# Performance work log

Hardware: AMD Instinct MI355X
Metric: run time of the kernel (lower is better)

The kernel has to match this reference:

```python
import jax, jax.numpy as jnp
import numpy as np

B, N, D = 2, 2048, 1024
H, WS = 16, 128  # num_heads, window_size
DH = D // H
HALF = WS // 2  # window is [i-HALF, i+HALF] inclusive -> 129 keys interior


def setup_inputs() -> dict:
    key = jax.random.key(0)
    ks = jax.random.split(key, 5)
    return {
        "x": jax.random.normal(ks[0], (B, N, D), dtype=jnp.float32),
        "Wqkv": jax.random.normal(ks[1], (D, 3 * D), dtype=jnp.float32) * 0.02,
        "bqkv": jax.random.normal(ks[2], (3 * D,), dtype=jnp.float32) * 0.02,
        "Wout": jax.random.normal(ks[3], (D, D), dtype=jnp.float32) * 0.02,
        "bout": jax.random.normal(ks[4], (D,), dtype=jnp.float32) * 0.02,
    }


def reference(x, Wqkv, bqkv, Wout, bout):
    b, n, d = x.shape
    scale = DH ** -0.5
    qkv = x @ Wqkv + bqkv  # [b, n, 3d]
    q, k, v = jnp.split(qkv, 3, axis=-1)
    # [b, n, d] -> [b, h, n, dh]
    def heads(t):
        return t.reshape(b, n, H, DH).transpose(0, 2, 1, 3)
    q, k, v = heads(q), heads(k), heads(v)
    scores = jnp.einsum("bhid,bhjd->bhij", q, k) * scale  # [b, h, n, n]
    # per-token window [max(0,i-HALF), min(n,i+HALF+1)) == |i-j| <= HALF
    idx = jnp.arange(n)
    band = jnp.abs(idx[:, None] - idx[None, :]) <= HALF  # [n, n]
    neg = jnp.asarray(jnp.finfo(scores.dtype).min, scores.dtype)
    scores = jnp.where(band[None, None], scores, neg)
    attn = jax.nn.softmax(scores, axis=-1)
    out = jnp.einsum("bhij,bhjd->bhid", attn, v)  # [b, h, n, dh]
    out = out.transpose(0, 2, 1, 3).reshape(b, n, d)
    return out @ Wout + bout
```

## Files before the change

kernel.cpp:

```cpp
#include <hip/hip_runtime.h>
#include <hip/hip_bf16.h>
#include <cstdint>
#include <cstddef>

#define BB 2
#define NN 2048
#define DD 1024
#define HH 16
#define DHH 64
#define SCALE 0.125f

typedef _Float16 f16x8 __attribute__((ext_vector_type(8)));
typedef _Float16 f16x4 __attribute__((ext_vector_type(4)));
typedef float f32x4 __attribute__((ext_vector_type(4)));

#define AS1(p) ((__attribute__((address_space(1))) void*)(p))
#define AS3(p) ((__attribute__((address_space(3))) void*)(p))

__global__ __launch_bounds__(256) void prep(const float* __restrict__ x, _Float16* __restrict__ x_h,
                                            const float* __restrict__ Wqkv, _Float16* __restrict__ Wqkv_t,
                                            const float* __restrict__ Wout, _Float16* __restrict__ Wout_t) {
    __shared__ float tile[32][33];
    int bx = blockIdx.x, tid = threadIdx.x;
    if (bx < 2048) {
        int i = bx * 2048 + tid * 8;
        f32x4 a = *(const f32x4*)(x + i);
        f32x4 b = *(const f32x4*)(x + i + 4);
        f16x8 o;
        o[0] = (_Float16)a[0]; o[1] = (_Float16)a[1]; o[2] = (_Float16)a[2]; o[3] = (_Float16)a[3];
        o[4] = (_Float16)b[0]; o[5] = (_Float16)b[1]; o[6] = (_Float16)b[2]; o[7] = (_Float16)b[3];
        *(f16x8*)(x_h + i) = o;
        return;
    }
    const float* in; _Float16* out; int C, tc, tr;
    if (bx < 5120) { int t = bx - 2048; C = 3 * DD; in = Wqkv; out = Wqkv_t; tc = t % 96; tr = t / 96; }
    else           { int t = bx - 5120; C = DD;     in = Wout; out = Wout_t; tc = t % 32; tr = t / 32; }
    int R = DD;
    int txx = tid & 31, ty = tid >> 5;
    int r0 = tr * 32, c0 = tc * 32;
#pragma unroll
    for (int i = 0; i < 32; i += 8)
        tile[ty + i][txx] = in[(size_t)(r0 + ty + i) * C + (c0 + txx)];
    __syncthreads();
#pragma unroll
    for (int i = 0; i < 32; i += 8)
        out[(size_t)(c0 + ty + i) * R + (r0 + txx)] = (_Float16)tile[txx][ty + i];
}

template <bool SWAP, int MT>
__device__ __forceinline__ void gemm_kloop(const _Float16* __restrict__ gA,
                                           const _Float16* __restrict__ gB,
                                           _Float16* lA, _Float16* lB,
                                           const _Float16* As, const _Float16* Bs,
                                           int wm, int wn, int llo, int lhi, int K,
                                           f32x4 acc[][MT > 4 ? MT : 4]) {
    for (int k0 = 0; k0 < K; k0 += 64) {
        __syncthreads();
#pragma unroll
        for (int p = 0; p < MT; ++p)
            __builtin_amdgcn_global_load_lds(AS1(gA + (size_t)p * 8 * K + k0), AS3(lA + p * 512), 16, 0, 0);
#pragma unroll
        for (int p = 0; p < 4; ++p)
            __builtin_amdgcn_global_load_lds(AS1(gB + (size_t)p * 8 * K + k0), AS3(lB + p * 512), 16, 0, 0);
        __syncthreads();

#pragma unroll
        for (int ks = 0; ks < 2; ++ks) {
            f16x8 af[MT], bf[4];
            int swz = (((ks * 4 + lhi) ^ (llo & 7)) * 8);
#pragma unroll
            for (int mt = 0; mt < MT; ++mt)
                af[mt] = *(const f16x8*)(As + (wm + mt * 16 + llo) * 64 + swz);
#pragma unroll
            for (int nt = 0; nt < 4; ++nt)
                bf[nt] = *(const f16x8*)(Bs + (wn + nt * 16 + llo) * 64 + swz);
            if (SWAP) {
#pragma unroll
                for (int nt = 0; nt < 4; ++nt)
#pragma unroll
                    for (int mt = 0; mt < MT; ++mt)
                        acc[nt][mt] = __builtin_amdgcn_mfma_f32_16x16x32_f16(bf[nt], af[mt], acc[nt][mt], 0, 0, 0);
            } else {
#pragma unroll
                for (int mt = 0; mt < MT; ++mt)
#pragma unroll
                    for (int nt = 0; nt < 4; ++nt)
                        acc[mt][nt] = __builtin_amdgcn_mfma_f32_16x16x32_f16(af[mt], bf[nt], acc[mt][nt], 0, 0, 0);
            }
        }
    }
}

template <bool SWAP>
__device__ __forceinline__ void qkv_body(const _Float16* __restrict__ A,
                                         const _Float16* __restrict__ Bt,
                                         const float* __restrict__ bias,
                                         _Float16* __restrict__ q_h,
                                         _Float16* __restrict__ k_h,
                                         _Float16* __restrict__ vt_h,
                                         _Float16* As, _Float16* Bs,
                                         int bm, int bn, int region) {
    (void)region;
    int tid = threadIdx.x;
    int wave = tid >> 6, lane = tid & 63;
    int llo = lane & 15, lhi = lane >> 4;
    int wm = (wave >> 2) * 128, wn = (wave & 3) * 64;
    int l8 = lane >> 3;
    int gchunk = ((lane & 7) ^ l8) * 8;

    int rAu = wm + (wave & 3) * 16;
    int rBu = (wave >> 1) * 64 + (wave & 1) * 16;
    const _Float16* gA = A + (size_t)(bm + rAu + l8) * DD + gchunk;
    const _Float16* gB = Bt + (size_t)(bn + rBu + l8) * DD + gchunk;
    _Float16* lA = As + rAu * 64 + lane * 8;
    _Float16* lB = Bs + rBu * 64 + lane * 8;

#define STA(H, C, T, U) __builtin_amdgcn_global_load_lds( \
        AS1(gA + (size_t)((H) * 64 + (C) * 8) * DD + (T) * 64), \
        AS3(lA + (U) * 16384 + ((H) * 64 + (C) * 8) * 64), 16, 0, 0)
#define STB(H, C, T, U) __builtin_amdgcn_global_load_lds( \
        AS1(gB + (size_t)((H) * 32 + (C) * 8) * DD + (T) * 64), \
        AS3(lB + (U) * 16384 + ((H) * 32 + (C) * 8) * 64), 16, 0, 0)
#define RDA(MT, KS, U) (*(const f16x8*)(As + (U) * 16384 + (wm + (MT) * 16 + llo) * 64 + ((((KS) * 4 + lhi) ^ (llo & 7)) * 8)))
#define RDB(NT, KS, U) (*(const f16x8*)(Bs + (U) * 16384 + (wn + (NT) * 16 + llo) * 64 + ((((KS) * 4 + lhi) ^ (llo & 7)) * 8)))
#define MM(MT, NT, KS) do { \
        if constexpr (SWAP) acc[NT][MT] = __builtin_amdgcn_mfma_f32_16x16x32_f16(bf[NT][KS], af[(MT) & 3][KS], acc[NT][MT], 0, 0, 0); \
        else acc[MT][NT] = __builtin_amdgcn_mfma_f32_16x16x32_f16(af[(MT) & 3][KS], bf[NT][KS], acc[MT][NT], 0, 0, 0); \
    } while (0)

    f32x4 acc[SWAP ? 4 : 8][SWAP ? 8 : 4] = {};
    f16x8 af[4][2], bf[4][2];

    STA(0, 0, 0, 0); STA(0, 1, 0, 0);
    STB(0, 0, 0, 0); STB(0, 1, 0, 0);
    STB(1, 0, 0, 0); STB(1, 1, 0, 0);
    STA(1, 0, 0, 0); STA(1, 1, 0, 0);
    asm volatile("s_waitcnt vmcnt(4)" ::: "memory");
    __builtin_amdgcn_s_barrier();

#pragma unroll 1
    for (int t = 0; t < 15; ++t) {
        int u = t & 1, nu = u ^ 1;
#pragma unroll
        for (int mt = 0; mt < 4; ++mt) { af[mt][0] = RDA(mt, 0, u); af[mt][1] = RDA(mt, 1, u); }
#pragma unroll
        for (int nt = 0; nt < 2; ++nt) { bf[nt][0] = RDB(nt, 0, u); bf[nt][1] = RDB(nt, 1, u); }
        STA(0, 0, t + 1, nu); STA(0, 1, t + 1, nu);
        STB(0, 0, t + 1, nu); STB(0, 1, t + 1, nu);
        __builtin_amdgcn_s_barrier();
        asm volatile("s_waitcnt lgkmcnt(0)" ::: "memory");
        __builtin_amdgcn_s_setprio(1);
#pragma unroll
        for (int ks = 0; ks < 2; ++ks)
#pragma unroll
            for (int mt = 0; mt < 4; ++mt) { MM(mt, 0, ks); MM(mt, 1, ks); }
        __builtin_amdgcn_s_setprio(0);
        asm volatile("s_waitcnt vmcnt(6)" ::: "memory");
        __builtin_amdgcn_s_barrier();
#pragma unroll
        for (int nt = 2; nt < 4; ++nt) { bf[nt][0] = RDB(nt, 0, u); bf[nt][1] = RDB(nt, 1, u); }
        STB(1, 0, t + 1, nu); STB(1, 1, t + 1, nu);
        __builtin_amdgcn_s_barrier();
        asm volatile("s_waitcnt lgkmcnt(0)" ::: "memory");
        __builtin_amdgcn_s_setprio(1);
#pragma unroll
        for (int ks = 0; ks < 2; ++ks)
#pragma unroll
            for (int mt = 0; mt < 4; ++mt) { MM(mt, 2, ks); MM(mt, 3, ks); }
        __builtin_amdgcn_s_setprio(0);
        asm volatile("s_waitcnt vmcnt(6)" ::: "memory");
        __builtin_amdgcn_s_barrier();
#pragma unroll
        for (int mt = 0; mt < 4; ++mt) { af[mt][0] = RDA(mt + 4, 0, u); af[mt][1] = RDA(mt + 4, 1, u); }
        STA(1, 0, t + 1, nu); STA(1, 1, t + 1, nu);
        __builtin_amdgcn_s_barrier();
        asm volatile("s_waitcnt lgkmcnt(0)" ::: "memory");
        __builtin_amdgcn_s_setprio(1);
#pragma unroll
        for (int ks = 0; ks < 2; ++ks)
#pragma unroll
            for (int mt = 4; mt < 8; ++mt) { MM(mt, 2, ks); MM(mt, 3, ks); }
        __builtin_amdgcn_s_setprio(0);
        __builtin_amdgcn_s_barrier();
        __builtin_amdgcn_s_setprio(1);
#pragma unroll
        for (int ks = 0; ks < 2; ++ks)
#pragma unroll
            for (int mt = 4; mt < 8; ++mt) { MM(mt, 0, ks); MM(mt, 1, ks); }
        __builtin_amdgcn_s_setprio(0);
        asm volatile("s_waitcnt vmcnt(4)" ::: "memory");
        __builtin_amdgcn_s_barrier();
    }

    {
#pragma unroll
        for (int mt = 0; mt < 4; ++mt) { af[mt][0] = RDA(mt, 0, 1); af[mt][1] = RDA(mt, 1, 1); }
#pragma unroll
        for (int nt = 0; nt < 2; ++nt) { bf[nt][0] = RDB(nt, 0, 1); bf[nt][1] = RDB(nt, 1, 1); }
        asm volatile("s_waitcnt lgkmcnt(0)" ::: "memory");
        __builtin_amdgcn_s_setprio(1);
#pragma unroll
        for (int ks = 0; ks < 2; ++ks)
#pragma unroll
            for (int mt = 0; mt < 4; ++mt) { MM(mt, 0, ks); MM(mt, 1, ks); }
        __builtin_amdgcn_s_setprio(0);
        asm volatile("s_waitcnt vmcnt(2)" ::: "memory");
        __builtin_amdgcn_s_barrier();
#pragma unroll
        for (int nt = 2; nt < 4; ++nt) { bf[nt][0] = RDB(nt, 0, 1); bf[nt][1] = RDB(nt, 1, 1); }
        asm volatile("s_waitcnt lgkmcnt(0)" ::: "memory");
        __builtin_amdgcn_s_setprio(1);
#pragma unroll
        for (int ks = 0; ks < 2; ++ks)
#pragma unroll
            for (int mt = 0; mt < 4; ++mt) { MM(mt, 2, ks); MM(mt, 3, ks); }
        __builtin_amdgcn_s_setprio(0);
        asm volatile("s_waitcnt vmcnt(0)" ::: "memory");
        __builtin_amdgcn_s_barrier();
#pragma unroll
        for (int mt = 0; mt < 4; ++mt) { af[mt][0] = RDA(mt + 4, 0, 1); af[mt][1] = RDA(mt + 4, 1, 1); }
        asm volatile("s_waitcnt lgkmcnt(0)" ::: "memory");
        __builtin_amdgcn_s_setprio(1);
#pragma unroll
        for (int ks = 0; ks < 2; ++ks)
#pragma unroll
            for (int mt = 4; mt < 8; ++mt) { MM(mt, 0, ks); MM(mt, 1, ks); MM(mt, 2, ks); MM(mt, 3, ks); }
        __builtin_amdgcn_s_setprio(0);
    }

    if constexpr (SWAP) {
        _Float16* dst0 = (region == 0 ? q_h : k_h);
#pragma unroll
        for (int nt = 0; nt < 4; ++nt) {
            int cbase = bn + wn + nt * 16 + lhi * 4;
            f32x4 b4 = *(const f32x4*)(bias + cbase);
            int c = cbase & 1023;
#pragma unroll
            for (int mt = 0; mt < 8; ++mt) {
                int tkn = bm + wm + mt * 16 + llo;
                int b = tkn >> 11, n = tkn & 2047;
                f16x4 v4;
#pragma unroll
                for (int r = 0; r < 4; ++r) v4[r] = (_Float16)(acc[nt][mt][r] + b4[r]);
                *(f16x4*)(dst0 + (size_t)(b * NN + n) * DD + c) = v4;
            }
        }
    } else {
#pragma unroll
        for (int nt = 0; nt < 4; ++nt) {
            int col = bn + wn + nt * 16 + llo;
            float bv = bias[col];
            int c = col & 1023;
            int h = c >> 6, dh = c & 63;
#pragma unroll
            for (int mt = 0; mt < 8; ++mt) {
                int row = bm + wm + mt * 16 + lhi * 4;
                int b = row >> 11, n = row & 2047;
                f16x4 v4;
#pragma unroll
                for (int r = 0; r < 4; ++r) v4[r] = (_Float16)(acc[mt][nt][r] + bv);
                *(f16x4*)(vt_h + ((size_t)((b * HH + h) * DHH + dh)) * NN + n) = v4;
            }
        }
    }
#undef STA
#undef STB
#undef RDA
#undef RDB
#undef MM
}

__global__ __launch_bounds__(512, 2) void gemm_qkv(const _Float16* __restrict__ A,
                                                   const _Float16* __restrict__ Bt,
                                                   const float* __restrict__ bias,
                                                   _Float16* __restrict__ q_h,
                                                   _Float16* __restrict__ k_h,
                                                   _Float16* __restrict__ vt_h) {
    __shared__ __align__(16) _Float16 As[2 * 16384];
    __shared__ __align__(16) _Float16 Bs[2 * 16384];
    int id = blockIdx.x;
    int xcd = id & 7, jj = id >> 3;
    int mtile = (xcd >> 1) * 4 + jj / 6;
    int ntile = (xcd & 1) * 6 + jj % 6;
    int bm = mtile * 256, bn = ntile * 256;
    int region = bn >> 10;
    if (region == 2)
        qkv_body<false>(A, Bt, bias, q_h, k_h, vt_h, As, Bs, bm, bn, region);
    else
        qkv_body<true>(A, Bt, bias, q_h, k_h, vt_h, As, Bs, bm, bn, region);
}

__global__ __launch_bounds__(256) void gemm_out(const _Float16* __restrict__ A,
                                                const _Float16* __restrict__ Bt,
                                                const float* __restrict__ bias,
                                                float* __restrict__ Cf) {
    const int K = DD, N = DD;
    __shared__ __align__(16) _Float16 As[64 * 64];
    __shared__ __align__(16) _Float16 Bs[128 * 64];
    int id = blockIdx.x;
    int xcd = id & 7, j = id >> 3;
    int bm = (xcd * 8 + (j >> 3)) * 64;
    int bn = (j & 7) * 128;
    int tid = threadIdx.x;
    int wave = tid >> 6, lane = tid & 63;
    int wm = (wave >> 1) * 32, wn = (wave & 1) * 64;
    int lhi = lane >> 4, llo = lane & 15;

    f32x4 acc[4][4] = {};

    int srowA = wave * 16 + (lane >> 3);
    int srowB = wave * 32 + (lane >> 3);
    int scol = ((lane & 7) ^ (lane >> 3)) * 8;
    const _Float16* gA = A + (size_t)(bm + srowA) * K + scol;
    const _Float16* gB = Bt + (size_t)(bn + srowB) * K + scol;
    _Float16* lA = As + wave * 1024 + lane * 8;
    _Float16* lB = Bs + wave * 2048 + lane * 8;

    gemm_kloop<true, 2>(gA, gB, lA, lB, As, Bs, wm, wn, llo, lhi, K,
                        (f32x4(*)[4])acc);

#pragma unroll
    for (int nt = 0; nt < 4; ++nt) {
        int cbase = bn + wn + nt * 16 + lhi * 4;
        f32x4 b4 = *(const f32x4*)(bias + cbase);
#pragma unroll
        for (int mt = 0; mt < 2; ++mt) {
            int t = bm + wm + mt * 16 + llo;
            f32x4 v4;
#pragma unroll
            for (int r = 0; r < 4; ++r) v4[r] = acc[nt][mt][r] + b4[r];
            *(f32x4*)(Cf + (size_t)t * N + cbase) = v4;
        }
    }
}

#define KP 64
#define PP 200
#define VP 200
__global__ __launch_bounds__(256) void local_attn(const _Float16* __restrict__ q_h,
                                                  const _Float16* __restrict__ k_h,
                                                  const _Float16* __restrict__ vt_h,
                                                  _Float16* __restrict__ outh) {
    __shared__ __align__(16) _Float16 KsPs[64 * PP];
    __shared__ __align__(16) _Float16 Vt[64 * VP];
    _Float16* Ks = KsPs;
    _Float16* Ps = KsPs;
    int tid = threadIdx.x;
    int id = blockIdx.x;
    int xcd = id & 7, j = id >> 3;
    int i0 = (xcd * 4 + (j & 3)) * 64;
    int hb = j >> 2;
    int h = hb & 15, b = hb >> 4;

    int wave = tid >> 6, lane = tid & 63;
    int llo = lane & 15, lhi = lane >> 4;

    {
        int srow = lane >> 3;
        int chunk = ((lane & 7) ^ (lane >> 3)) * 8;
        const _Float16* kb = k_h + (size_t)(b * NN) * DD + h * DHH + chunk;
#pragma unroll
        for (int q = 0; q < 6; ++q) {
            int p = wave * 6 + q;
            int jj = i0 - 64 + p * 8 + srow;
            __builtin_amdgcn_global_load_lds(AS1(kb + (ptrdiff_t)jj * DD), AS3(Ks + p * 512 + lane * 8), 16, 0, 0);
        }
    }

    {
        const _Float16* vb = vt_h + (size_t)((b * HH + h) * DHH) * NN + (i0 - 64);
        for (int u = tid; u < 1536; u += 256) {
            int d = u / 24, c = u % 24;
            f16x8 vv = *(const f16x8*)(vb + (ptrdiff_t)d * NN + c * 8);
            *(f16x8*)(Vt + d * VP + c * 8) = vv;
        }
    }

    int qrow = wave * 16 + llo;
    int qi = i0 + qrow;
    const _Float16* qp = q_h + (size_t)(b * NN + qi) * DD + h * DHH;
    f16x8 qf0 = *(const f16x8*)(qp + lhi * 8);
    f16x8 qf1 = *(const f16x8*)(qp + 32 + lhi * 8);
    __syncthreads();

    float sc[12][4];
#pragma unroll
    for (int mt = 0; mt < 12; ++mt) {
        const _Float16* kr = Ks + (mt * 16 + llo) * 64;
        f16x8 kf0 = *(const f16x8*)(kr + ((lhi ^ (llo & 7)) * 8));
        f16x8 kf1 = *(const f16x8*)(kr + (((lhi + 4) ^ (llo & 7)) * 8));
        f32x4 a = {0.f, 0.f, 0.f, 0.f};
        a = __builtin_amdgcn_mfma_f32_16x16x32_f16(kf0, qf0, a, 0, 0, 0);
        a = __builtin_amdgcn_mfma_f32_16x16x32_f16(kf1, qf1, a, 0, 0, 0);
#pragma unroll
        for (int r = 0; r < 4; ++r) sc[mt][r] = a[r];
    }
    __syncthreads();

    float m = -1e30f;
#pragma unroll
    for (int mt = 0; mt < 12; ++mt)
#pragma unroll
        for (int r = 0; r < 4; ++r) {
            int sidx = mt * 16 + lhi * 4 + r;
            int jj = i0 - 64 + sidx;
            int dj = jj - qi;
            bool valid = (jj >= 0) && (jj < NN) && (dj <= 64) && (dj >= -64);
            float v = valid ? sc[mt][r] * SCALE : -1e30f;
            sc[mt][r] = v;
            m = fmaxf(m, v);
        }
    m = fmaxf(m, __shfl_xor(m, 16, 64));
    m = fmaxf(m, __shfl_xor(m, 32, 64));
    float l = 0.f;
#pragma unroll
    for (int mt = 0; mt < 12; ++mt)
#pragma unroll
        for (int r = 0; r < 4; ++r) {
            float e = __expf(sc[mt][r] - m);
            sc[mt][r] = e;
            l += e;
        }
    l += __shfl_xor(l, 16, 64);
    l += __shfl_xor(l, 32, 64);
    float invl = 1.f / l;

#pragma unroll
    for (int mt = 0; mt < 12; ++mt) {
        f16x4 pv;
#pragma unroll
        for (int r = 0; r < 4; ++r) pv[r] = (_Float16)(sc[mt][r] * invl);
        *(f16x4*)(Ps + qrow * PP + mt * 16 + lhi * 4) = pv;
    }
    __asm__ volatile("s_waitcnt lgkmcnt(0)" ::: "memory");

    f32x4 oacc[4] = {};
#pragma unroll
    for (int ks = 0; ks < 6; ++ks) {
        f16x8 pf = *(const f16x8*)(Ps + (wave * 16 + llo) * PP + ks * 32 + lhi * 8);
#pragma unroll
        for (int nt = 0; nt < 4; ++nt) {
            f16x8 vf = *(const f16x8*)(Vt + (nt * 16 + llo) * VP + ks * 32 + lhi * 8);
            oacc[nt] = __builtin_amdgcn_mfma_f32_16x16x32_f16(pf, vf, oacc[nt], 0, 0, 0);
        }
    }

    _Float16* orow = outh + (size_t)(b * NN) * DD + h * DHH;
#pragma unroll
    for (int nt = 0; nt < 4; ++nt)
#pragma unroll
        for (int r = 0; r < 4; ++r) {
            int q = wave * 16 + lhi * 4 + r;
            int d = nt * 16 + llo;
            orow[(size_t)(i0 + q) * DD + d] = (_Float16)oacc[nt][r];
        }
}

extern "C" void kernel_launch(void* const* d_in, const int* in_sizes, int n_in,
                              void* d_out, int out_size, void* d_ws, size_t ws_size,
                              hipStream_t stream) {
    const float* x    = (const float*)d_in[0];
    const float* Wqkv = (const float*)d_in[1];
    const float* bqkv = (const float*)d_in[2];
    const float* Wout = (const float*)d_in[3];
    const float* bout = (const float*)d_in[4];
    float* out = (float*)d_out;

    char* ws = (char*)d_ws;
    _Float16* x_h    = (_Float16*)(ws);
    _Float16* Wqkv_t = (_Float16*)(ws + (size_t)8  * 1024 * 1024);
    _Float16* Wout_t = (_Float16*)(ws + (size_t)14 * 1024 * 1024);
    _Float16* q_h    = (_Float16*)(ws + (size_t)16 * 1024 * 1024);
    _Float16* k_h    = (_Float16*)(ws + (size_t)24 * 1024 * 1024);
    _Float16* vt_h   = (_Float16*)(ws + (size_t)32 * 1024 * 1024);
    _Float16* attn_h = (_Float16*)(ws + (size_t)40 * 1024 * 1024);

    prep<<<6144, 256, 0, stream>>>(x, x_h, Wqkv, Wqkv_t, Wout, Wout_t);

    gemm_qkv<<<192, 512, 0, stream>>>(x_h, Wqkv_t, bqkv, q_h, k_h, vt_h);

    local_attn<<<1024, 256, 0, stream>>>(q_h, k_h, vt_h, attn_h);

    gemm_out<<<512, 256, 0, stream>>>(attn_h, Wout_t, bout, out);
}
```

Baseline: 152.7 us.

## Enlarge local attention to 128-query blocks with per-wave band skipping; 128x128 out GEMM tiles

```diff
diff --git a/kernel.cpp b/kernel.cpp
--- a/kernel.cpp
+++ b/kernel.cpp
@@ -295,36 +295,34 @@
                                                 const float* __restrict__ bias,
                                                 float* __restrict__ Cf) {
     const int K = DD, N = DD;
-    __shared__ __align__(16) _Float16 As[64 * 64];
+    __shared__ __align__(16) _Float16 As[128 * 64];
     __shared__ __align__(16) _Float16 Bs[128 * 64];
     int id = blockIdx.x;
     int xcd = id & 7, j = id >> 3;
-    int bm = (xcd * 8 + (j >> 3)) * 64;
+    int bm = (xcd * 4 + (j >> 3)) * 128;
     int bn = (j & 7) * 128;
     int tid = threadIdx.x;
     int wave = tid >> 6, lane = tid & 63;
-    int wm = (wave >> 1) * 32, wn = (wave & 1) * 64;
+    int wm = (wave >> 1) * 64, wn = (wave & 1) * 64;
     int lhi = lane >> 4, llo = lane & 15;
 
     f32x4 acc[4][4] = {};
 
-    int srowA = wave * 16 + (lane >> 3);
-    int srowB = wave * 32 + (lane >> 3);
+    int srow = wave * 32 + (lane >> 3);
     int scol = ((lane & 7) ^ (lane >> 3)) * 8;
-    const _Float16* gA = A + (size_t)(bm + srowA) * K + scol;
-    const _Float16* gB = Bt + (size_t)(bn + srowB) * K + scol;
-    _Float16* lA = As + wave * 1024 + lane * 8;
+    const _Float16* gA = A + (size_t)(bm + srow) * K + scol;
+    const _Float16* gB = Bt + (size_t)(bn + srow) * K + scol;
+    _Float16* lA = As + wave * 2048 + lane * 8;
     _Float16* lB = Bs + wave * 2048 + lane * 8;
 
-    gemm_kloop<true, 2>(gA, gB, lA, lB, As, Bs, wm, wn, llo, lhi, K,
-                        (f32x4(*)[4])acc);
+    gemm_kloop<true, 4>(gA, gB, lA, lB, As, Bs, wm, wn, llo, lhi, K, acc);
 
 #pragma unroll
     for (int nt = 0; nt < 4; ++nt) {
         int cbase = bn + wn + nt * 16 + lhi * 4;
         f32x4 b4 = *(const f32x4*)(bias + cbase);
 #pragma unroll
-        for (int mt = 0; mt < 2; ++mt) {
+        for (int mt = 0; mt < 4; ++mt) {
             int t = bm + wm + mt * 16 + llo;
             f32x4 v4;
 #pragma unroll
@@ -334,22 +332,21 @@
     }
 }
 
-#define KP 64
-#define PP 200
-#define VP 200
-__global__ __launch_bounds__(256) void local_attn(const _Float16* __restrict__ q_h,
-                                                  const _Float16* __restrict__ k_h,
-                                                  const _Float16* __restrict__ vt_h,
-                                                  _Float16* __restrict__ outh) {
-    __shared__ __align__(16) _Float16 KsPs[64 * PP];
-    __shared__ __align__(16) _Float16 Vt[64 * VP];
+#define PP2 168
+#define VP2 280
+__global__ __launch_bounds__(512, 4) void local_attn(const _Float16* __restrict__ q_h,
+                                                     const _Float16* __restrict__ k_h,
+                                                     const _Float16* __restrict__ vt_h,
+                                                     _Float16* __restrict__ outh) {
+    __shared__ __align__(16) _Float16 KsPs[128 * PP2];
+    __shared__ __align__(16) _Float16 Vt[64 * VP2];
     _Float16* Ks = KsPs;
     _Float16* Ps = KsPs;
     int tid = threadIdx.x;
     int id = blockIdx.x;
     int xcd = id & 7, j = id >> 3;
-    int i0 = (xcd * 4 + (j & 3)) * 64;
-    int hb = j >> 2;
+    int i0 = (xcd * 2 + (j & 1)) * 128;
+    int hb = j >> 1;
     int h = hb & 15, b = hb >> 4;
 
     int wave = tid >> 6, lane = tid & 63;
@@ -360,8 +357,8 @@
         int chunk = ((lane & 7) ^ (lane >> 3)) * 8;
         const _Float16* kb = k_h + (size_t)(b * NN) * DD + h * DHH + chunk;
 #pragma unroll
-        for (int q = 0; q < 6; ++q) {
-            int p = wave * 6 + q;
+        for (int q = 0; q < 4; ++q) {
+            int p = wave * 4 + q;
             int jj = i0 - 64 + p * 8 + srow;
             __builtin_amdgcn_global_load_lds(AS1(kb + (ptrdiff_t)jj * DD), AS3(Ks + p * 512 + lane * 8), 16, 0, 0);
         }
@@ -369,10 +366,16 @@
 
     {
         const _Float16* vb = vt_h + (size_t)((b * HH + h) * DHH) * NN + (i0 - 64);
-        for (int u = tid; u < 1536; u += 256) {
-            int d = u / 24, c = u % 24;
+#pragma unroll
+        for (int u = tid; u < 2048; u += 512) {
+            int d = u >> 5, c = u & 31;
             f16x8 vv = *(const f16x8*)(vb + (ptrdiff_t)d * NN + c * 8);
-            *(f16x8*)(Vt + d * VP + c * 8) = vv;
+            *(f16x8*)(Vt + d * VP2 + c * 8) = vv;
+        }
+        if (tid < 192) {
+            int d = tid / 3, c = tid % 3;
+            f16x8 z = {};
+            *(f16x8*)(Vt + d * VP2 + 256 + c * 8) = z;
         }
     }
 
@@ -383,42 +386,42 @@
     f16x8 qf1 = *(const f16x8*)(qp + 32 + lhi * 8);
     __syncthreads();
 
-    float sc[12][4];
-#pragma unroll
-    for (int mt = 0; mt < 12; ++mt) {
-        const _Float16* kr = Ks + (mt * 16 + llo) * 64;
+    float sc[9][4];
+#pragma unroll
+    for (int mtl = 0; mtl < 9; ++mtl) {
+        const _Float16* kr = Ks + ((wave + mtl) * 16 + llo) * 64;
         f16x8 kf0 = *(const f16x8*)(kr + ((lhi ^ (llo & 7)) * 8));
         f16x8 kf1 = *(const f16x8*)(kr + (((lhi + 4) ^ (llo & 7)) * 8));
         f32x4 a = {0.f, 0.f, 0.f, 0.f};
         a = __builtin_amdgcn_mfma_f32_16x16x32_f16(kf0, qf0, a, 0, 0, 0);
         a = __builtin_amdgcn_mfma_f32_16x16x32_f16(kf1, qf1, a, 0, 0, 0);
 #pragma unroll
-        for (int r = 0; r < 4; ++r) sc[mt][r] = a[r];
+        for (int r = 0; r < 4; ++r) sc[mtl][r] = a[r];
     }
     __syncthreads();
 
     float m = -1e30f;
 #pragma unroll
-    for (int mt = 0; mt < 12; ++mt)
+    for (int mtl = 0; mtl < 9; ++mtl)
 #pragma unroll
         for (int r = 0; r < 4; ++r) {
-            int sidx = mt * 16 + lhi * 4 + r;
+            int sidx = (wave + mtl) * 16 + lhi * 4 + r;
             int jj = i0 - 64 + sidx;
             int dj = jj - qi;
             bool valid = (jj >= 0) && (jj < NN) && (dj <= 64) && (dj >= -64);
-            float v = valid ? sc[mt][r] * SCALE : -1e30f;
-            sc[mt][r] = v;
+            float v = valid ? sc[mtl][r] * SCALE : -1e30f;
+            sc[mtl][r] = v;
             m = fmaxf(m, v);
         }
     m = fmaxf(m, __shfl_xor(m, 16, 64));
     m = fmaxf(m, __shfl_xor(m, 32, 64));
     float l = 0.f;
 #pragma unroll
-    for (int mt = 0; mt < 12; ++mt)
+    for (int mtl = 0; mtl < 9; ++mtl)
 #pragma unroll
         for (int r = 0; r < 4; ++r) {
-            float e = __expf(sc[mt][r] - m);
-            sc[mt][r] = e;
+            float e = __expf(sc[mtl][r] - m);
+            sc[mtl][r] = e;
             l += e;
         }
     l += __shfl_xor(l, 16, 64);
@@ -426,21 +429,25 @@
     float invl = 1.f / l;
 
 #pragma unroll
-    for (int mt = 0; mt < 12; ++mt) {
+    for (int mtl = 0; mtl < 9; ++mtl) {
         f16x4 pv;
 #pragma unroll
-        for (int r = 0; r < 4; ++r) pv[r] = (_Float16)(sc[mt][r] * invl);
-        *(f16x4*)(Ps + qrow * PP + mt * 16 + lhi * 4) = pv;
+        for (int r = 0; r < 4; ++r) pv[r] = (_Float16)(sc[mtl][r] * invl);
+        *(f16x4*)(Ps + qrow * PP2 + mtl * 16 + lhi * 4) = pv;
+    }
+    {
+        f16x4 z4 = {};
+        *(f16x4*)(Ps + qrow * PP2 + 144 + lhi * 4) = z4;
     }
     __asm__ volatile("s_waitcnt lgkmcnt(0)" ::: "memory");
 
     f32x4 oacc[4] = {};
 #pragma unroll
-    for (int ks = 0; ks < 6; ++ks) {
-        f16x8 pf = *(const f16x8*)(Ps + (wave * 16 + llo) * PP + ks * 32 + lhi * 8);
+    for (int ks = 0; ks < 5; ++ks) {
+        f16x8 pf = *(const f16x8*)(Ps + qrow * PP2 + ks * 32 + lhi * 8);
 #pragma unroll
         for (int nt = 0; nt < 4; ++nt) {
-            f16x8 vf = *(const f16x8*)(Vt + (nt * 16 + llo) * VP + ks * 32 + lhi * 8);
+            f16x8 vf = *(const f16x8*)(Vt + (nt * 16 + llo) * VP2 + wave * 16 + ks * 32 + lhi * 8);
             oacc[nt] = __builtin_amdgcn_mfma_f32_16x16x32_f16(pf, vf, oacc[nt], 0, 0, 0);
         }
     }
@@ -479,7 +486,7 @@
 
     gemm_qkv<<<192, 512, 0, stream>>>(x_h, Wqkv_t, bqkv, q_h, k_h, vt_h);
 
-    local_attn<<<1024, 256, 0, stream>>>(q_h, k_h, vt_h, attn_h);
-
-    gemm_out<<<512, 256, 0, stream>>>(attn_h, Wout_t, bout, out);
-}
+    local_attn<<<512, 512, 0, stream>>>(q_h, k_h, vt_h, attn_h);
+
+    gemm_out<<<256, 256, 0, stream>>>(attn_h, Wout_t, bout, out);
+}
```

After: 152.6 us. Within noise of the previous version (-0.1%).

## Stage QKV epilogue through swizzled LDS for wide stores; enlarge out-GEMM tile

Applied to the files above, without the earlier changes.

```diff
diff --git a/kernel.cpp b/kernel.cpp
--- a/kernel.cpp
+++ b/kernel.cpp
@@ -180,9 +180,6 @@
         for (int ks = 0; ks < 2; ++ks)
 #pragma unroll
             for (int mt = 4; mt < 8; ++mt) { MM(mt, 2, ks); MM(mt, 3, ks); }
-        __builtin_amdgcn_s_setprio(0);
-        __builtin_amdgcn_s_barrier();
-        __builtin_amdgcn_s_setprio(1);
 #pragma unroll
         for (int ks = 0; ks < 2; ++ks)
 #pragma unroll
@@ -228,39 +225,62 @@
         __builtin_amdgcn_s_setprio(0);
     }
 
+    __builtin_amdgcn_s_barrier();
+    _Float16* R = (wave < 4) ? (As + wave * 8192) : (Bs + (wave - 4) * 8192);
+    int bq = bm >> 11;
+    int nb = (bm & 2047) + wm;
+
     if constexpr (SWAP) {
+#pragma unroll
+        for (int nt = 0; nt < 4; ++nt) {
+            int fb = nt * 16 + lhi * 4;
+            f32x4 b4 = *(const f32x4*)(bias + bn + wn + fb);
+            int chunk = fb >> 3, off = fb & 7;
+#pragma unroll
+            for (int mt = 0; mt < 8; ++mt) {
+                int t = mt * 16 + llo;
+                f16x4 v4;
+#pragma unroll
+                for (int r = 0; r < 4; ++r) v4[r] = (_Float16)(acc[nt][mt][r] + b4[r]);
+                *(f16x4*)(R + t * 64 + ((chunk ^ (t & 7)) << 3) + off) = v4;
+            }
+        }
+        asm volatile("s_waitcnt lgkmcnt(0)" ::: "memory");
         _Float16* dst0 = (region == 0 ? q_h : k_h);
+        int cb = (bn & 1023) + wn;
+#pragma unroll
+        for (int it = 0; it < 16; ++it) {
+            int t = it * 8 + l8;
+            f16x8 v = *(const f16x8*)(R + t * 64 + (((lane & 7) ^ (t & 7)) << 3));
+            *(f16x8*)(dst0 + (size_t)(bq * NN + nb + t) * DD + cb + (lane & 7) * 8) = v;
+        }
+    } else {
 #pragma unroll
         for (int nt = 0; nt < 4; ++nt) {
-            int cbase = bn + wn + nt * 16 + lhi * 4;
-            f32x4 b4 = *(const f32x4*)(bias + cbase);
-            int c = cbase & 1023;
+            int f = nt * 16 + llo;
+            float bv = bias[bn + wn + f];
 #pragma unroll
             for (int mt = 0; mt < 8; ++mt) {
-                int tkn = bm + wm + mt * 16 + llo;
-                int b = tkn >> 11, n = tkn & 2047;
+                int tb = mt * 16 + lhi * 4;
+                int chunk = tb >> 3, off = tb & 7;
+                int slot = (chunk & 8) | ((chunk & 7) ^ (f & 7));
                 f16x4 v4;
 #pragma unroll
-                for (int r = 0; r < 4; ++r) v4[r] = (_Float16)(acc[nt][mt][r] + b4[r]);
-                *(f16x4*)(dst0 + (size_t)(b * NN + n) * DD + c) = v4;
+                for (int r = 0; r < 4; ++r) v4[r] = (_Float16)(acc[mt][nt][r] + bv);
+                *(f16x4*)(R + f * 128 + (slot << 3) + off) = v4;
             }
         }
-    } else {
-#pragma unroll
-        for (int nt = 0; nt < 4; ++nt) {
-            int col = bn + wn + nt * 16 + llo;
-            float bv = bias[col];
-            int c = col & 1023;
+        asm volatile("s_waitcnt lgkmcnt(0)" ::: "memory");
+        int cb = (bn & 1023) + wn;
+#pragma unroll
+        for (int it = 0; it < 16; ++it) {
+            int f = it * 4 + lhi;
+            int chunk = llo;
+            int slot = (chunk & 8) | ((chunk & 7) ^ (f & 7));
+            f16x8 v = *(const f16x8*)(R + f * 128 + (slot << 3));
+            int c = cb + f;
             int h = c >> 6, dh = c & 63;
-#pragma unroll
-            for (int mt = 0; mt < 8; ++mt) {
-                int row = bm + wm + mt * 16 + lhi * 4;
-                int b = row >> 11, n = row & 2047;
-                f16x4 v4;
-#pragma unroll
-                for (int r = 0; r < 4; ++r) v4[r] = (_Float16)(acc[mt][nt][r] + bv);
-                *(f16x4*)(vt_h + ((size_t)((b * HH + h) * DHH + dh)) * NN + n) = v4;
-            }
+            *(f16x8*)(vt_h + ((size_t)((bq * HH + h) * DHH + dh)) * NN + nb + chunk * 8) = v;
         }
     }
 #undef STA
@@ -295,36 +315,34 @@
                                                 const float* __restrict__ bias,
                                                 float* __restrict__ Cf) {
     const int K = DD, N = DD;
-    __shared__ __align__(16) _Float16 As[64 * 64];
+    __shared__ __align__(16) _Float16 As[128 * 64];
     __shared__ __align__(16) _Float16 Bs[128 * 64];
     int id = blockIdx.x;
     int xcd = id & 7, j = id >> 3;
-    int bm = (xcd * 8 + (j >> 3)) * 64;
+    int bm = (xcd * 4 + (j >> 3)) * 128;
     int bn = (j & 7) * 128;
     int tid = threadIdx.x;
     int wave = tid >> 6, lane = tid & 63;
-    int wm = (wave >> 1) * 32, wn = (wave & 1) * 64;
+    int wm = (wave >> 1) * 64, wn = (wave & 1) * 64;
     int lhi = lane >> 4, llo = lane & 15;
 
     f32x4 acc[4][4] = {};
 
-    int srowA = wave * 16 + (lane >> 3);
-    int srowB = wave * 32 + (lane >> 3);
+    int srow = wave * 32 + (lane >> 3);
     int scol = ((lane & 7) ^ (lane >> 3)) * 8;
-    const _Float16* gA = A + (size_t)(bm + srowA) * K + scol;
-    const _Float16* gB = Bt + (size_t)(bn + srowB) * K + scol;
-    _Float16* lA = As + wave * 1024 + lane * 8;
+    const _Float16* gA = A + (size_t)(bm + srow) * K + scol;
+    const _Float16* gB = Bt + (size_t)(bn + srow) * K + scol;
+    _Float16* lA = As + wave * 2048 + lane * 8;
     _Float16* lB = Bs + wave * 2048 + lane * 8;
 
-    gemm_kloop<true, 2>(gA, gB, lA, lB, As, Bs, wm, wn, llo, lhi, K,
-                        (f32x4(*)[4])acc);
+    gemm_kloop<true, 4>(gA, gB, lA, lB, As, Bs, wm, wn, llo, lhi, K, acc);
 
 #pragma unroll
     for (int nt = 0; nt < 4; ++nt) {
         int cbase = bn + wn + nt * 16 + lhi * 4;
         f32x4 b4 = *(const f32x4*)(bias + cbase);
 #pragma unroll
-        for (int mt = 0; mt < 2; ++mt) {
+        for (int mt = 0; mt < 4; ++mt) {
             int t = bm + wm + mt * 16 + llo;
             f32x4 v4;
 #pragma unroll
@@ -481,5 +499,5 @@
 
     local_attn<<<1024, 256, 0, stream>>>(q_h, k_h, vt_h, attn_h);
 
-    gemm_out<<<512, 256, 0, stream>>>(attn_h, Wout_t, bout, out);
-}
+    gemm_out<<<256, 256, 0, stream>>>(attn_h, Wout_t, bout, out);
+}
```

Result: no change. 152.4 us (-0.2%).
